# Kernel optimization log

Measured on AMD Instinct MI355X. Metric: run time of the kernel, lower is better.

The kernel has to match this reference:

```python
import jax, jax.numpy as jnp
import numpy as np

K = 20

def lrelu(x):
    return jnp.where(x >= 0, x, 0.2 * x)

def get_graph_feature(x, k):
    # x: (B, N, C) channel-last. Returns (B, N, k, 2C) = [neighbor - x, x].
    inner = jnp.einsum('bnc,bmc->bnm', x, x)          # (B, N, N)
    sq = jnp.sum(x * x, axis=-1)                       # (B, N)
    # negative squared distance; top-k gives nearest neighbors (incl. self)
    neg_dist = 2.0 * inner - sq[:, :, None] - sq[:, None, :]
    _, idx = jax.lax.top_k(neg_dist, k)                # (B, N, k)
    neigh = jnp.take_along_axis(x[:, None, :, :], idx[:, :, :, None], axis=2)  # (B, N, k, C)
    center = jnp.broadcast_to(x[:, :, None, :], neigh.shape)
    return jnp.concatenate([neigh - center, center], axis=-1)

def setup_inputs() -> dict:
    key = jax.random.key(0)
    ks = jax.random.split(key, 12)
    B, N, input_dim = 32, 2048, 6
    emb_dim, out_dim = 1024, 40
    def w(k_, shape):
        fan_in = shape[-1]
        return jax.random.normal(k_, shape, dtype=jnp.float32) * (1.0 / np.sqrt(fan_in))
    return {
        'x':  jax.random.normal(ks[0], (B, N, input_dim), dtype=jnp.float32),
        'W1': w(ks[1], (64, 6)),            # conv1: 1x1 conv, no bias
        'W2': w(ks[2], (64, 128)),          # conv2
        'W5': w(ks[3], (emb_dim, 128)),     # conv5 (1d)
        'W3': w(ks[4], (32, input_dim - 3)),# conv3
        'W4': w(ks[5], (64, 32)),           # conv4
        'L1': w(ks[6], (128, (emb_dim + 64) * 2)),  # linear1, no bias
        'L2w': w(ks[7], (64, 128)),
        'L2b': jnp.zeros((64,), dtype=jnp.float32),
        'L3w': w(ks[8], (out_dim, 64)),
        'L3b': jnp.zeros((out_dim,), dtype=jnp.float32),
    }

def reference(x, W1, W2, W5, W3, W4, L1, L2w, L2b, L3w, L3b):
    x_pos = x[:, :, :3]       # (B, N, 3)
    x_feat = x[:, :, 3:]      # (B, N, input_dim-3)

    # EdgeConv block 1
    e = get_graph_feature(x_pos, K)                       # (B, N, k, 6)
    e = lrelu(jnp.einsum('bnkc,oc->bnko', e, W1))         # (B, N, k, 64)
    x1 = jnp.max(e, axis=2)                               # (B, N, 64)

    # EdgeConv block 2
    e = get_graph_feature(x1, K)                          # (B, N, k, 128)
    e = lrelu(jnp.einsum('bnkc,oc->bnko', e, W2))         # (B, N, k, 64)
    x2 = jnp.max(e, axis=2)                               # (B, N, 64)

    # conv5 over concatenated features
    h = jnp.concatenate([x1, x2], axis=-1)                # (B, N, 128)
    h = lrelu(jnp.einsum('bnc,oc->bno', h, W5))           # (B, N, emb)
    g = jnp.concatenate([jnp.max(h, axis=1), jnp.mean(h, axis=1)], axis=-1)  # (B, 2*emb)

    # per-point feature MLP (conv3 -> conv4)
    f = lrelu(jnp.einsum('bnc,oc->bno', x_feat, W3))      # (B, N, 32)
    f = lrelu(jnp.einsum('bnc,oc->bno', f, W4))           # (B, N, 64)
    fg = jnp.concatenate([jnp.max(f, axis=1), jnp.mean(f, axis=1)], axis=-1)  # (B, 128)

    z = jnp.concatenate([g, fg], axis=-1)                 # (B, (emb+64)*2)
    z = lrelu(z @ L1.T)
    z = lrelu(z @ L2w.T + L2b)
    return z @ L3w.T + L3b                                # (B, output)
```

## Files before the change

### kernel.cpp

```cpp
#include <hip/hip_runtime.h>
#include <math.h>

#define B_ 32
#define N_ 2048
#define KNN 20
#define FINF 3.402823466e38f
#define SCAP 256

typedef __attribute__((ext_vector_type(8))) short short8;
typedef __attribute__((ext_vector_type(4))) float f32x4;

#define OFF_X1   ((size_t)0)
#define OFF_X2   (OFF_X1 + (size_t)B_*N_*64*4)
#define OFF_SQ1  (OFF_X2 + (size_t)B_*N_*64*4)
#define OFF_IDX1 (OFF_SQ1 + (size_t)B_*N_*4)
#define OFF_IDX2 (OFF_IDX1 + (size_t)B_*N_*KNN*4)
#define OFF_PMAX (OFF_IDX2 + (size_t)B_*N_*KNN*4)
#define OFF_PSUM (OFF_PMAX + (size_t)B_*16*1024*4)
#define OFF_G    (OFF_PSUM + (size_t)B_*16*1024*4)
#define OFF_FG   (OFF_G + (size_t)B_*2048*4)
#define OFF_DIST (OFF_FG + (size_t)B_*128*4)
#define OFF_BASE OFF_DIST
#define OFF_XHI  (OFF_BASE + (size_t)B_*N_*64*4)
#define OFF_XLO  (OFF_XHI + (size_t)B_*N_*128*2)
#define OFF_WHI  (OFF_XLO + (size_t)B_*N_*128*2)
#define OFF_WLO  (OFF_WHI + (size_t)1024*128*2)

__device__ __forceinline__ float lrelu(float x) { return x >= 0.0f ? x : 0.2f * x; }

template<class F>
__device__ __forceinline__ void wave_top20_slow(const float (&v)[32], int lane, int* out20, F idxf) {
    unsigned alive = 0xffffffffu;
    for (int sel = 0; sel < 20; ++sel) {
        float bv = -FINF;
        int bm = 0x7fffffff;
#pragma unroll
        for (int j = 0; j < 32; ++j) {
            bool a = (alive >> j) & 1u;
            bool better = a && (v[j] > bv);
            bv = better ? v[j] : bv;
            bm = better ? idxf(j) : bm;
        }
#pragma unroll
        for (int off = 32; off; off >>= 1) {
            float ov = __shfl_xor(bv, off, 64);
            int   om = __shfl_xor(bm, off, 64);
            bool take = (ov > bv) || (ov == bv && om < bm);
            bv = take ? ov : bv;
            bm = take ? om : bm;
        }
        if (lane == 0) out20[sel] = bm;
#pragma unroll
        for (int j = 0; j < 32; ++j)
            if (idxf(j) == bm) alive &= ~(1u << j);
    }
}

template<class F>
__device__ __forceinline__ void wave_top20_fast(const float (&v)[32], int lane,
                                                float* sval, int* sidx, int* out20, F idxf) {
    float lm = v[0];
#pragma unroll
    for (int j = 1; j < 32; ++j) lm = fmaxf(lm, v[j]);
    float s = lm;
#pragma unroll
    for (int k = 2; k <= 64; k <<= 1) {
#pragma unroll
        for (int j2 = k >> 1; j2 > 0; j2 >>= 1) {
            float o = __shfl_xor(s, j2, 64);
            bool up = ((lane & k) == 0);
            bool high = ((lane & j2) != 0);
            s = (high == up) ? fmaxf(s, o) : fminf(s, o);
        }
    }
    float that = __shfl(s, 44, 64);
    int cnt = 0;
    unsigned long long below = (lane == 63) ? 0xffffffffffffffffull >> 1
                                            : ((1ull << lane) - 1ull);
#pragma unroll
    for (int j = 0; j < 32; ++j) {
        bool p = (v[j] >= that);
        unsigned long long mk = __ballot(p);
        if (p) {
            int slot = cnt + (int)__popcll(mk & below);
            if (slot < SCAP) { sval[slot] = v[j]; sidx[slot] = idxf(j); }
        }
        cnt += (int)__popcll(mk);
    }
    int S = cnt;
    if (S > SCAP) {
        wave_top20_slow(v, lane, out20, idxf);
        return;
    }
    if (S <= 64) {
        bool ok = lane < S;
        float cv = ok ? sval[lane] : -FINF;
        int   cm = ok ? sidx[lane] : 0x7fffffff;
#pragma unroll
        for (int k = 2; k <= 64; k <<= 1) {
#pragma unroll
            for (int j2 = k >> 1; j2 > 0; j2 >>= 1) {
                float ov = __shfl_xor(cv, j2, 64);
                int   om = __shfl_xor(cm, j2, 64);
                bool up = ((lane & k) == 0);
                bool high = ((lane & j2) != 0);
                bool cur_first = (cv > ov) || (cv == ov && cm < om);
                bool take = (high == up) ? cur_first : !cur_first;
                cv = take ? ov : cv;
                cm = take ? om : cm;
            }
        }
        if (lane < 20) out20[lane] = cm;
    } else {
        float cv[4]; int cm[4]; unsigned alive = 0;
#pragma unroll
        for (int r = 0; r < 4; ++r) {
            int i = r * 64 + lane;
            bool ok = i < S;
            float vv = sval[i];
            int   mm = sidx[i];
            cv[r] = ok ? vv : -FINF;
            cm[r] = ok ? mm : 0x7fffffff;
            if (ok) alive |= 1u << r;
        }
        for (int sel = 0; sel < 20; ++sel) {
            float bv = -FINF; int bm = 0x7fffffff;
#pragma unroll
            for (int r = 0; r < 4; ++r) {
                bool a = (alive >> r) & 1u;
                bool better = a && (cv[r] > bv || (cv[r] == bv && cm[r] < bm));
                bv = better ? cv[r] : bv;
                bm = better ? cm[r] : bm;
            }
#pragma unroll
            for (int off = 32; off; off >>= 1) {
                float ov = __shfl_xor(bv, off, 64);
                int   om = __shfl_xor(bm, off, 64);
                bool take = (ov > bv) || (ov == bv && om < bm);
                bv = take ? ov : bv;
                bm = take ? om : bm;
            }
            if (lane == 0) out20[sel] = bm;
#pragma unroll
            for (int r = 0; r < 4; ++r)
                if (cm[r] == bm) alive &= ~(1u << r);
        }
    }
}

__global__ __launch_bounds__(256) void k1_knn_pos(const float* __restrict__ x,
                                                  int* __restrict__ idx1) {
    __shared__ float sP[N_ * 3];
    __shared__ float sval[4][SCAP];
    __shared__ int   sidx[4][SCAP];
    __shared__ int   sOut[4][20];
    int tid = threadIdx.x;
    int wid = tid >> 6, lane = tid & 63;
    int row = blockIdx.x * 4 + wid;
    int b = row >> 11, n = row & 2047;
    const float* xb = x + (size_t)b * N_ * 6;
    for (int m = tid; m < N_; m += 256) {
        float4 f = *(const float4*)(xb + m * 6);
        sP[m*3+0] = f.x; sP[m*3+1] = f.y; sP[m*3+2] = f.z;
    }
    __syncthreads();
    float cx = sP[n*3+0], cy = sP[n*3+1], cz = sP[n*3+2];
    float sqn = cx*cx + cy*cy + cz*cz;
    float v[32];
#pragma unroll
    for (int j = 0; j < 32; ++j) {
        int m = lane + (j << 6);
        float mx_ = sP[m*3+0], my = sP[m*3+1], mz = sP[m*3+2];
        float inner = cx*mx_ + cy*my + cz*mz;
        float sqm = mx_*mx_ + my*my + mz*mz;
        v[j] = 2.0f*inner - sqn - sqm;
    }
    wave_top20_fast(v, lane, sval[wid], sidx[wid], sOut[wid],
                    [lane](int j) { return lane + (j << 6); });
    __syncthreads();
    if (lane < 20) idx1[(size_t)row*KNN + lane] = sOut[wid][lane];
}

__global__ __launch_bounds__(256) void k2_conv1(const float* __restrict__ x,
                                                const int* __restrict__ idx1,
                                                const float* __restrict__ W1,
                                                float* __restrict__ x1,
                                                float* __restrict__ sq1) {
    int wid = threadIdx.x >> 6, o = threadIdx.x & 63;
    int row = blockIdx.x * 4 + wid;
    int b = row >> 11, n = row & 2047;
    const float* xb = x + (size_t)b * N_ * 6;
    float w0 = W1[o*6+0], w1 = W1[o*6+1], w2 = W1[o*6+2];
    float w3 = W1[o*6+3], w4 = W1[o*6+4], w5 = W1[o*6+5];
    float cx = xb[n*6+0], cy = xb[n*6+1], cz = xb[n*6+2];
    float base = w3*cx + w4*cy + w5*cz;
    float mx = -FINF;
    for (int k = 0; k < KNN; ++k) {
        int m = idx1[(size_t)row*KNN + k];
        float dx = xb[m*6+0]-cx, dy = xb[m*6+1]-cy, dz = xb[m*6+2]-cz;
        float s = base + w0*dx + w1*dy + w2*dz;
        s = lrelu(s);
        mx = fmaxf(mx, s);
    }
    x1[(size_t)row*64 + o] = mx;
    float sq = mx*mx;
#pragma unroll
    for (int off = 32; off; off >>= 1) sq += __shfl_xor(sq, off, 64);
    if (o == 0) sq1[row] = sq;
}

__global__ __launch_bounds__(256) void k3_dist(const float* __restrict__ x1,
                                               const float* __restrict__ sq1,
                                               float* __restrict__ dist, int b0) {
    __shared__ float sA[32][128];
    __shared__ float sB[32][128];
    int t = blockIdx.x;
    int I = (int)((sqrtf(8.0f*t + 1.0f) - 1.0f) * 0.5f);
    while ((I+1)*(I+2)/2 <= t) ++I;
    while (I*(I+1)/2 > t) --I;
    int J = t - I*(I+1)/2;
    int b = b0 + blockIdx.y;
    const float* Xb  = x1  + (size_t)b * N_ * 64;
    const float* sqb = sq1 + (size_t)b * N_;
    float* Db = dist + (size_t)blockIdx.y * N_ * N_;
    int i0 = I*128, j0 = J*128;
    int tid = threadIdx.x;
    float acc[8][8] = {};
    for (int kt = 0; kt < 64; kt += 32) {
#pragma unroll
        for (int l = 0; l < 4; ++l) {
            int v = l*256 + tid;
            int i = v >> 3, cg = (v & 7) << 2;
            float4 fa = *(const float4*)(Xb + (size_t)(i0+i)*64 + kt + cg);
            sA[cg+0][i] = fa.x; sA[cg+1][i] = fa.y; sA[cg+2][i] = fa.z; sA[cg+3][i] = fa.w;
            float4 fb = *(const float4*)(Xb + (size_t)(j0+i)*64 + kt + cg);
            sB[cg+0][i] = fb.x; sB[cg+1][i] = fb.y; sB[cg+2][i] = fb.z; sB[cg+3][i] = fb.w;
        }
        __syncthreads();
        int ti = (tid & 15) * 8, tj = (tid >> 4) * 8;
#pragma unroll 4
        for (int c = 0; c < 32; ++c) {
            float a[8], w[8];
            *(float4*)&a[0] = *(const float4*)&sA[c][ti];
            *(float4*)&a[4] = *(const float4*)&sA[c][ti+4];
            *(float4*)&w[0] = *(const float4*)&sB[c][tj];
            *(float4*)&w[4] = *(const float4*)&sB[c][tj+4];
#pragma unroll
            for (int ii = 0; ii < 8; ++ii)
#pragma unroll
                for (int jj = 0; jj < 8; ++jj)
                    acc[ii][jj] = fmaf(a[ii], w[jj], acc[ii][jj]);
        }
        __syncthreads();
    }
    int ti = (tid & 15) * 8, tj = (tid >> 4) * 8;
    float sqi[8], sqj[8];
#pragma unroll
    for (int ii = 0; ii < 8; ++ii) sqi[ii] = sqb[i0 + ti + ii];
#pragma unroll
    for (int jj = 0; jj < 8; ++jj) sqj[jj] = sqb[j0 + tj + jj];
#pragma unroll
    for (int ii = 0; ii < 8; ++ii) {
        float ov[8];
#pragma unroll
        for (int jj = 0; jj < 8; ++jj) ov[jj] = 2.0f*acc[ii][jj] - sqi[ii] - sqj[jj];
        float4* p = (float4*)(Db + (size_t)(i0+ti+ii)*N_ + j0 + tj);
        p[0] = *(float4*)&ov[0]; p[1] = *(float4*)&ov[4];
    }
    if (I != J) {
#pragma unroll
        for (int jj = 0; jj < 8; ++jj) {
            float ov[8];
#pragma unroll
            for (int ii = 0; ii < 8; ++ii) ov[ii] = 2.0f*acc[ii][jj] - sqi[ii] - sqj[jj];
            float4* p = (float4*)(Db + (size_t)(j0+tj+jj)*N_ + i0 + ti);
            p[0] = *(float4*)&ov[0]; p[1] = *(float4*)&ov[4];
        }
    }
}

__global__ __launch_bounds__(256) void k4_topk(const float* __restrict__ dist,
                                               int* __restrict__ idx2, int b0) {
    __shared__ float sval[4][SCAP];
    __shared__ int   sidx[4][SCAP];
    __shared__ int   sOut[4][20];
    int wid = threadIdx.x >> 6, lane = threadIdx.x & 63;
    int lrow = blockIdx.x * 4 + wid;
    int lb = lrow >> 11, n = lrow & 2047;
    const float4* Dr4 = (const float4*)(dist + (size_t)lb * N_ * N_ + (size_t)n * N_);
    float v[32];
#pragma unroll
    for (int j4 = 0; j4 < 8; ++j4) {
        float4 f = Dr4[(j4 << 6) + lane];
        v[j4*4+0] = f.x; v[j4*4+1] = f.y; v[j4*4+2] = f.z; v[j4*4+3] = f.w;
    }
    wave_top20_fast(v, lane, sval[wid], sidx[wid], sOut[wid],
                    [lane](int j) { return (lane << 2) + ((j >> 2) << 8) + (j & 3); });
    __syncthreads();
    int row = (b0 + lb) * N_ + n;
    if (lane < 20) idx2[(size_t)row*KNN + lane] = sOut[wid][lane];
}

__global__ __launch_bounds__(256) void k5pre_base(const float* __restrict__ x1,
                                                  const float* __restrict__ W2,
                                                  float* __restrict__ base) {
    int w = threadIdx.x >> 6, o = threadIdx.x & 63;
    float wreg[64];
    const float* wsrc = W2 + (size_t)o * 128 + 64;
#pragma unroll
    for (int j = 0; j < 16; ++j)
        *(float4*)&wreg[j*4] = *(const float4*)(wsrc + j*4);
    int row0 = (blockIdx.x * 4 + w) * 32;
    for (int r = 0; r < 32; ++r) {
        const float* xr = x1 + (size_t)(row0 + r) * 64;
        float acc = 0.0f;
#pragma unroll
        for (int j = 0; j < 16; ++j) {
            float4 xc = *(const float4*)(xr + j*4);
            acc = fmaf(wreg[j*4+0], xc.x, acc);
            acc = fmaf(wreg[j*4+1], xc.y, acc);
            acc = fmaf(wreg[j*4+2], xc.z, acc);
            acc = fmaf(wreg[j*4+3], xc.w, acc);
        }
        base[(size_t)(row0 + r) * 64 + o] = acc;
    }
}

__global__ __launch_bounds__(256) void k5_conv2(const float* __restrict__ x1,
                                                const int* __restrict__ idx2,
                                                const float* __restrict__ W2,
                                                const float* __restrict__ base,
                                                float* __restrict__ x2) {
    __shared__ float sWT[64][64];
    __shared__ float sD[4][20][66];
    int tid = threadIdx.x;
    int w = tid >> 6, lane = tid & 63;
    int row = blockIdx.x * 4 + w;
    int b = row >> 11, n = row & 2047;
    const float* Xb = x1 + (size_t)b * N_ * 64;
    {
        int o = tid & 63, chunk = tid >> 6;
        int c0 = chunk * 16;
        const float* src = W2 + (size_t)o * 128 + c0;
#pragma unroll
        for (int j = 0; j < 4; ++j) {
            float4 f = *(const float4*)(src + j * 4);
            int c = c0 + j * 4;
            sWT[c+0][o] = f.x; sWT[c+1][o] = f.y; sWT[c+2][o] = f.z; sWT[c+3][o] = f.w;
        }
    }
    const float* cen = Xb + (size_t)n * 64;
#pragma unroll
    for (int it = 0; it < 5; ++it) {
        int task = lane + it * 64;
        int k = task >> 4, c4 = (task & 15) * 4;
        int m = idx2[(size_t)row * KNN + k];
        float4 nb = *(const float4*)(Xb + (size_t)m * 64 + c4);
        float4 ce = *(const float4*)(cen + c4);
        float4 d;
        d.x = nb.x - ce.x; d.y = nb.y - ce.y; d.z = nb.z - ce.z; d.w = nb.w - ce.w;
        *(float4*)&sD[w][k][c4] = d;
    }
    __syncthreads();
    int og = lane & 15, kg = lane >> 4;
    int o0 = og * 4;
    float4 bs = *(const float4*)(base + (size_t)row * 64 + o0);
    float bb[4] = {bs.x, bs.y, bs.z, bs.w};
    float acc[5][4] = {};
    for (int c4 = 0; c4 < 64; c4 += 4) {
        float wv[4][4];
#pragma unroll
        for (int ci = 0; ci < 4; ++ci)
            *(float4*)wv[ci] = *(const float4*)&sWT[c4 + ci][o0];
        float dv[5][4];
#pragma unroll
        for (int ki = 0; ki < 5; ++ki)
            *(float4*)dv[ki] = *(const float4*)&sD[w][kg * 5 + ki][c4];
#pragma unroll
        for (int ki = 0; ki < 5; ++ki)
#pragma unroll
            for (int ci = 0; ci < 4; ++ci)
#pragma unroll
                for (int oi = 0; oi < 4; ++oi)
                    acc[ki][oi] = fmaf(dv[ki][ci], wv[ci][oi], acc[ki][oi]);
    }
    float res[4];
#pragma unroll
    for (int oi = 0; oi < 4; ++oi) {
        float m = -FINF;
#pragma unroll
        for (int ki = 0; ki < 5; ++ki)
            m = fmaxf(m, lrelu(bb[oi] + acc[ki][oi]));
        m = fmaxf(m, __shfl_xor(m, 16, 64));
        m = fmaxf(m, __shfl_xor(m, 32, 64));
        res[oi] = m;
    }
    if (kg == 0) {
        float4 o4; o4.x = res[0]; o4.y = res[1]; o4.z = res[2]; o4.w = res[3];
        *(float4*)(x2 + (size_t)row * 64 + o0) = o4;
    }
}

__global__ __launch_bounds__(256) void k6pre_split(const float* __restrict__ x1,
                                                   const float* __restrict__ x2,
                                                   const float* __restrict__ W5,
                                                   unsigned short* __restrict__ Xhi,
                                                   unsigned short* __restrict__ Xlo,
                                                   unsigned short* __restrict__ Whi,
                                                   unsigned short* __restrict__ Wlo) {
    const int NX = B_ * N_ * 128 / 4;
    int e4 = blockIdx.x * 256 + threadIdx.x;
    float4 v;
    unsigned short* dh; unsigned short* dl; size_t doff;
    if (e4 < NX) {
        int r = e4 >> 5, c4 = (e4 & 31) << 2;
        v = (c4 < 64) ? *(const float4*)(x1 + (size_t)r*64 + c4)
                      : *(const float4*)(x2 + (size_t)r*64 + (c4 - 64));
        dh = Xhi; dl = Xlo; doff = (size_t)r*128 + c4;
    } else {
        int e = e4 - NX;
        if (e >= 1024*128/4) return;
        int r = e >> 5, c4 = (e & 31) << 2;
        v = *(const float4*)(W5 + (size_t)r*128 + c4);
        dh = Whi; dl = Wlo; doff = (size_t)r*128 + c4;
    }
    float a[4] = {v.x, v.y, v.z, v.w};
    unsigned short hh[4], ll[4];
#pragma unroll
    for (int i = 0; i < 4; ++i) {
        unsigned u = __float_as_uint(a[i]);
        unsigned r16 = (u + 0x7fffu + ((u >> 16) & 1u)) >> 16;
        hh[i] = (unsigned short)r16;
        float lo = a[i] - __uint_as_float(r16 << 16);
        unsigned ul = __float_as_uint(lo);
        ll[i] = (unsigned short)((ul + 0x7fffu + ((ul >> 16) & 1u)) >> 16);
    }
    *(uint2*)(dh + doff) = make_uint2((unsigned)hh[0] | ((unsigned)hh[1] << 16),
                                      (unsigned)hh[2] | ((unsigned)hh[3] << 16));
    *(uint2*)(dl + doff) = make_uint2((unsigned)ll[0] | ((unsigned)ll[1] << 16),
                                      (unsigned)ll[2] | ((unsigned)ll[3] << 16));
}

__global__ __launch_bounds__(256) void k6a_mfma(const unsigned short* __restrict__ Xhi,
                                                const unsigned short* __restrict__ Xlo,
                                                const unsigned short* __restrict__ Whi,
                                                const unsigned short* __restrict__ Wlo,
                                                float* __restrict__ pmax,
                                                float* __restrict__ psum) {
    __shared__ unsigned short sT[4][128*32];
    __shared__ float redmx[128][2], redsm[128][2];
    int tid = threadIdx.x;
    int nt = blockIdx.x >> 3, ot = blockIdx.x & 7, b = blockIdx.y;
    int wid = tid >> 6, lane = tid & 63;
    int wn = wid & 1, wo = wid >> 1;
    int sub = lane & 15, quad = lane >> 4;
    const unsigned short* gp[4];
    gp[0] = Xhi + (size_t)(b*2048 + nt*128) * 128;
    gp[1] = Xlo + (size_t)(b*2048 + nt*128) * 128;
    gp[2] = Whi + (size_t)(ot*128) * 128;
    gp[3] = Wlo + (size_t)(ot*128) * 128;
    f32x4 acc[4][4];
#pragma unroll
    for (int i = 0; i < 4; ++i)
#pragma unroll
        for (int j = 0; j < 4; ++j) acc[i][j] = (f32x4)0.0f;
    for (int kt = 0; kt < 4; ++kt) {
        int k0 = kt * 32;
        __syncthreads();
#pragma unroll
        for (int it = 0; it < 8; ++it) {
            int task = it*256 + tid;
            int tile = task >> 9, rem = task & 511;
            int row = rem >> 2, ch = rem & 3;
            uint4 d = *(const uint4*)(gp[tile] + (size_t)row*128 + k0 + ch*8);
            *(uint4*)(&sT[tile][row*32 + ch*8]) = d;
        }
        __syncthreads();
        short8 ah[4], al[4], bh[4], bl[4];
#pragma unroll
        for (int mi = 0; mi < 4; ++mi) {
            int r = wn*64 + mi*16 + sub;
            ah[mi] = *(const short8*)(&sT[0][r*32 + quad*8]);
            al[mi] = *(const short8*)(&sT[1][r*32 + quad*8]);
        }
#pragma unroll
        for (int ni = 0; ni < 4; ++ni) {
            int r = wo*64 + ni*16 + sub;
            bh[ni] = *(const short8*)(&sT[2][r*32 + quad*8]);
            bl[ni] = *(const short8*)(&sT[3][r*32 + quad*8]);
        }
#pragma unroll
        for (int mi = 0; mi < 4; ++mi)
#pragma unroll
            for (int ni = 0; ni < 4; ++ni) {
                acc[mi][ni] = __builtin_amdgcn_mfma_f32_16x16x32_bf16(ah[mi], bh[ni], acc[mi][ni], 0, 0, 0);
                acc[mi][ni] = __builtin_amdgcn_mfma_f32_16x16x32_bf16(ah[mi], bl[ni], acc[mi][ni], 0, 0, 0);
                acc[mi][ni] = __builtin_amdgcn_mfma_f32_16x16x32_bf16(al[mi], bh[ni], acc[mi][ni], 0, 0, 0);
            }
    }
#pragma unroll
    for (int ni = 0; ni < 4; ++ni) {
        float mx = -FINF, sm = 0.0f;
#pragma unroll
        for (int mi = 0; mi < 4; ++mi)
#pragma unroll
            for (int r = 0; r < 4; ++r) {
                float v = lrelu(acc[mi][ni][r]);
                mx = fmaxf(mx, v); sm += v;
            }
        mx = fmaxf(mx, __shfl_xor(mx, 16, 64));
        mx = fmaxf(mx, __shfl_xor(mx, 32, 64));
        sm += __shfl_xor(sm, 16, 64);
        sm += __shfl_xor(sm, 32, 64);
        if (quad == 0) {
            redmx[wo*64 + ni*16 + sub][wn] = mx;
            redsm[wo*64 + ni*16 + sub][wn] = sm;
        }
    }
    __syncthreads();
    if (tid < 128) {
        float mx = fmaxf(redmx[tid][0], redmx[tid][1]);
        float sm = redsm[tid][0] + redsm[tid][1];
        size_t po = ((size_t)b*16 + nt)*1024 + ot*128 + tid;
        pmax[po] = mx; psum[po] = sm;
    }
}

__global__ __launch_bounds__(256) void k6b_reduce(const float* __restrict__ pmax,
                                                  const float* __restrict__ psum,
                                                  float* __restrict__ g) {
    int t = blockIdx.x * 256 + threadIdx.x;
    int b = t >> 10, o = t & 1023;
    float mx = -FINF, sm = 0.0f;
    for (int i = 0; i < 16; ++i) {
        mx = fmaxf(mx, pmax[((size_t)b*16 + i)*1024 + o]);
        sm += psum[((size_t)b*16 + i)*1024 + o];
    }
    g[(size_t)b*2048 + o] = mx;
    g[(size_t)b*2048 + 1024 + o] = sm * (1.0f/2048.0f);
}

__global__ __launch_bounds__(256) void k7_feat(const float* __restrict__ x,
                                               const float* __restrict__ W3,
                                               const float* __restrict__ W4,
                                               float* __restrict__ fg) {
    __shared__ float rmx[16*256];
    __shared__ float rsm[16*256];
    int b = blockIdx.y, og = blockIdx.x;
    int o0 = og * 16;
    int tid = threadIdx.x;
    float mx[16], sm[16];
#pragma unroll
    for (int i = 0; i < 16; ++i) { mx[i] = -FINF; sm[i] = 0.0f; }
    for (int n = tid; n < N_; n += 256) {
        const float* xr = x + ((size_t)b*N_ + n)*6 + 3;
        float f0 = xr[0], f1 = xr[1], f2 = xr[2];
        float h1[32];
#pragma unroll
        for (int j = 0; j < 32; ++j) {
            float s = W3[j*3]*f0 + W3[j*3+1]*f1 + W3[j*3+2]*f2;
            h1[j] = lrelu(s);
        }
#pragma unroll
        for (int oi = 0; oi < 16; ++oi) {
            float s = 0.0f;
#pragma unroll
            for (int j = 0; j < 32; ++j) s = fmaf(W4[(o0+oi)*32 + j], h1[j], s);
            s = lrelu(s);
            mx[oi] = fmaxf(mx[oi], s); sm[oi] += s;
        }
    }
#pragma unroll
    for (int oi = 0; oi < 16; ++oi) { rmx[oi*256 + tid] = mx[oi]; rsm[oi*256 + tid] = sm[oi]; }
    __syncthreads();
    for (int s = 128; s > 0; s >>= 1) {
        if (tid < s) {
#pragma unroll
            for (int oi = 0; oi < 16; ++oi) {
                rmx[oi*256 + tid] = fmaxf(rmx[oi*256 + tid], rmx[oi*256 + tid + s]);
                rsm[oi*256 + tid] += rsm[oi*256 + tid + s];
            }
        }
        __syncthreads();
    }
    if (tid < 16) {
        fg[(size_t)b*128 + o0 + tid]      = rmx[tid*256];
        fg[(size_t)b*128 + 64 + o0 + tid] = rsm[tid*256] * (1.0f/2048.0f);
    }
}

__global__ __launch_bounds__(128) void k8_head(const float* __restrict__ g,
                                               const float* __restrict__ fg,
                                               const float* __restrict__ L1w,
                                               const float* __restrict__ L2w,
                                               const float* __restrict__ L2b,
                                               const float* __restrict__ L3w,
                                               const float* __restrict__ L3b,
                                               float* __restrict__ out) {
    __shared__ float sz[2176];
    __shared__ float s1[128];
    __shared__ float s2[64];
    int b = blockIdx.x, tid = threadIdx.x;
    for (int c = tid; c < 2048; c += 128) sz[c] = g[(size_t)b*2048 + c];
    if (tid < 128) sz[2048 + tid] = fg[(size_t)b*128 + tid];
    __syncthreads();
    {
        float a = 0.0f;
        const float* w = L1w + (size_t)tid * 2176;
        for (int c = 0; c < 2176; ++c) a = fmaf(w[c], sz[c], a);
        s1[tid] = lrelu(a);
    }
    __syncthreads();
    if (tid < 64) {
        float a = L2b[tid];
        for (int c = 0; c < 128; ++c) a = fmaf(L2w[tid*128 + c], s1[c], a);
        s2[tid] = lrelu(a);
    }
    __syncthreads();
    if (tid < 40) {
        float a = L3b[tid];
        for (int c = 0; c < 64; ++c) a = fmaf(L3w[tid*64 + c], s2[c], a);
        out[(size_t)b*40 + tid] = a;
    }
}

extern "C" void kernel_launch(void* const* d_in, const int* in_sizes, int n_in,
                              void* d_out, int out_size, void* d_ws, size_t ws_size,
                              hipStream_t stream) {
    const float* x   = (const float*)d_in[0];
    const float* W1  = (const float*)d_in[1];
    const float* W2  = (const float*)d_in[2];
    const float* W5  = (const float*)d_in[3];
    const float* W3  = (const float*)d_in[4];
    const float* W4  = (const float*)d_in[5];
    const float* L1w = (const float*)d_in[6];
    const float* L2w = (const float*)d_in[7];
    const float* L2b = (const float*)d_in[8];
    const float* L3w = (const float*)d_in[9];
    const float* L3b = (const float*)d_in[10];
    float* out = (float*)d_out;

    char* ws = (char*)d_ws;
    float* x1   = (float*)(ws + OFF_X1);
    float* x2   = (float*)(ws + OFF_X2);
    float* sq1  = (float*)(ws + OFF_SQ1);
    int*   idx1 = (int*)  (ws + OFF_IDX1);
    int*   idx2 = (int*)  (ws + OFF_IDX2);
    float* pmax = (float*)(ws + OFF_PMAX);
    float* psum = (float*)(ws + OFF_PSUM);
    float* g    = (float*)(ws + OFF_G);
    float* fg   = (float*)(ws + OFF_FG);
    float* dist = (float*)(ws + OFF_DIST);
    float* base = (float*)(ws + OFF_BASE);
    unsigned short* Xhi = (unsigned short*)(ws + OFF_XHI);
    unsigned short* Xlo = (unsigned short*)(ws + OFF_XLO);
    unsigned short* Whi = (unsigned short*)(ws + OFF_WHI);
    unsigned short* Wlo = (unsigned short*)(ws + OFF_WLO);

    size_t distBytes = (size_t)N_ * N_ * 4;
    size_t availB = (ws_size > OFF_DIST) ? (ws_size - OFF_DIST) : 0;
    int maxcb = (int)(availB / distBytes);
    int cb = 4;
    while (cb * 2 <= maxcb && cb * 2 <= 32) cb <<= 1;

    k1_knn_pos<<<16384, 256, 0, stream>>>(x, idx1);
    k2_conv1<<<16384, 256, 0, stream>>>(x, idx1, W1, x1, sq1);
    for (int b0 = 0; b0 < 32; b0 += cb) {
        k3_dist<<<dim3(136, cb), 256, 0, stream>>>(x1, sq1, dist, b0);
        k4_topk<<<cb * 512, 256, 0, stream>>>(dist, idx2, b0);
    }
    k5pre_base<<<512, 256, 0, stream>>>(x1, W2, base);
    k5_conv2<<<16384, 256, 0, stream>>>(x1, idx2, W2, base, x2);
    k6pre_split<<<8320, 256, 0, stream>>>(x1, x2, W5, Xhi, Xlo, Whi, Wlo);
    k6a_mfma<<<dim3(128, 32), 256, 0, stream>>>(Xhi, Xlo, Whi, Wlo, pmax, psum);
    k6b_reduce<<<128, 256, 0, stream>>>(pmax, psum, g);
    k7_feat<<<dim3(4, 32), 256, 0, stream>>>(x, W3, W4, fg);
    k8_head<<<32, 128, 0, stream>>>(g, fg, L1w, L2w, L2b, L3w, L3b, out);
}
```

Before: 977.5 us.

## Factor EdgeConv2 linear map into per-point P and Q before gathering

```diff
diff --git a/kernel.cpp b/kernel.cpp
--- a/kernel.cpp
+++ b/kernel.cpp
@@ -20,10 +20,11 @@
 #define OFF_G    (OFF_PSUM + (size_t)B_*16*1024*4)
 #define OFF_FG   (OFF_G + (size_t)B_*2048*4)
 #define OFF_DIST (OFF_FG + (size_t)B_*128*4)
-#define OFF_BASE OFF_DIST
-#define OFF_XHI  (OFF_BASE + (size_t)B_*N_*64*4)
-#define OFF_XLO  (OFF_XHI + (size_t)B_*N_*128*2)
-#define OFF_WHI  (OFF_XLO + (size_t)B_*N_*128*2)
+#define OFF_P    OFF_DIST
+#define OFF_Q    (OFF_P + (size_t)B_*N_*64*4)
+#define OFF_XHI  OFF_P
+#define OFF_XLO  OFF_Q
+#define OFF_WHI  (OFF_Q + (size_t)B_*N_*64*4)
 #define OFF_WLO  (OFF_WHI + (size_t)1024*128*2)
 
 __device__ __forceinline__ float lrelu(float x) { return x >= 0.0f ? x : 0.2f * x; }
@@ -301,104 +302,57 @@
     if (lane < 20) idx2[(size_t)row*KNN + lane] = sOut[wid][lane];
 }
 
-__global__ __launch_bounds__(256) void k5pre_base(const float* __restrict__ x1,
-                                                  const float* __restrict__ W2,
-                                                  float* __restrict__ base) {
+__global__ __launch_bounds__(256) void k5pre_pq(const float* __restrict__ x1,
+                                                const float* __restrict__ W2,
+                                                float* __restrict__ P,
+                                                float* __restrict__ Q) {
     int w = threadIdx.x >> 6, o = threadIdx.x & 63;
-    float wreg[64];
-    const float* wsrc = W2 + (size_t)o * 128 + 64;
-#pragma unroll
-    for (int j = 0; j < 16; ++j)
-        *(float4*)&wreg[j*4] = *(const float4*)(wsrc + j*4);
+    float wd[64], wc[64];
+    const float* wsrc = W2 + (size_t)o * 128;
+#pragma unroll
+    for (int j = 0; j < 16; ++j) {
+        float4 d = *(const float4*)(wsrc + j*4);
+        float4 c = *(const float4*)(wsrc + 64 + j*4);
+        wd[j*4+0] = d.x; wd[j*4+1] = d.y; wd[j*4+2] = d.z; wd[j*4+3] = d.w;
+        wc[j*4+0] = c.x - d.x; wc[j*4+1] = c.y - d.y; wc[j*4+2] = c.z - d.z; wc[j*4+3] = c.w - d.w;
+    }
     int row0 = (blockIdx.x * 4 + w) * 32;
     for (int r = 0; r < 32; ++r) {
         const float* xr = x1 + (size_t)(row0 + r) * 64;
-        float acc = 0.0f;
+        float p = 0.0f, q = 0.0f;
 #pragma unroll
         for (int j = 0; j < 16; ++j) {
             float4 xc = *(const float4*)(xr + j*4);
-            acc = fmaf(wreg[j*4+0], xc.x, acc);
-            acc = fmaf(wreg[j*4+1], xc.y, acc);
-            acc = fmaf(wreg[j*4+2], xc.z, acc);
-            acc = fmaf(wreg[j*4+3], xc.w, acc);
-        }
-        base[(size_t)(row0 + r) * 64 + o] = acc;
-    }
-}
-
-__global__ __launch_bounds__(256) void k5_conv2(const float* __restrict__ x1,
-                                                const int* __restrict__ idx2,
-                                                const float* __restrict__ W2,
-                                                const float* __restrict__ base,
-                                                float* __restrict__ x2) {
-    __shared__ float sWT[64][64];
-    __shared__ float sD[4][20][66];
-    int tid = threadIdx.x;
-    int w = tid >> 6, lane = tid & 63;
+            p = fmaf(wd[j*4+0], xc.x, p); q = fmaf(wc[j*4+0], xc.x, q);
+            p = fmaf(wd[j*4+1], xc.y, p); q = fmaf(wc[j*4+1], xc.y, q);
+            p = fmaf(wd[j*4+2], xc.z, p); q = fmaf(wc[j*4+2], xc.z, q);
+            p = fmaf(wd[j*4+3], xc.w, p); q = fmaf(wc[j*4+3], xc.w, q);
+        }
+        P[(size_t)(row0 + r) * 64 + o] = p;
+        Q[(size_t)(row0 + r) * 64 + o] = q;
+    }
+}
+
+__global__ __launch_bounds__(256) void k5b_max(const float* __restrict__ P,
+                                               const float* __restrict__ Q,
+                                               const int* __restrict__ idx2,
+                                               float* __restrict__ x2) {
+    int w = threadIdx.x >> 6, lane = threadIdx.x & 63;
     int row = blockIdx.x * 4 + w;
-    int b = row >> 11, n = row & 2047;
-    const float* Xb = x1 + (size_t)b * N_ * 64;
-    {
-        int o = tid & 63, chunk = tid >> 6;
-        int c0 = chunk * 16;
-        const float* src = W2 + (size_t)o * 128 + c0;
-#pragma unroll
-        for (int j = 0; j < 4; ++j) {
-            float4 f = *(const float4*)(src + j * 4);
-            int c = c0 + j * 4;
-            sWT[c+0][o] = f.x; sWT[c+1][o] = f.y; sWT[c+2][o] = f.z; sWT[c+3][o] = f.w;
-        }
-    }
-    const float* cen = Xb + (size_t)n * 64;
-#pragma unroll
-    for (int it = 0; it < 5; ++it) {
-        int task = lane + it * 64;
-        int k = task >> 4, c4 = (task & 15) * 4;
-        int m = idx2[(size_t)row * KNN + k];
-        float4 nb = *(const float4*)(Xb + (size_t)m * 64 + c4);
-        float4 ce = *(const float4*)(cen + c4);
-        float4 d;
-        d.x = nb.x - ce.x; d.y = nb.y - ce.y; d.z = nb.z - ce.z; d.w = nb.w - ce.w;
-        *(float4*)&sD[w][k][c4] = d;
-    }
-    __syncthreads();
-    int og = lane & 15, kg = lane >> 4;
-    int o0 = og * 4;
-    float4 bs = *(const float4*)(base + (size_t)row * 64 + o0);
-    float bb[4] = {bs.x, bs.y, bs.z, bs.w};
-    float acc[5][4] = {};
-    for (int c4 = 0; c4 < 64; c4 += 4) {
-        float wv[4][4];
-#pragma unroll
-        for (int ci = 0; ci < 4; ++ci)
-            *(float4*)wv[ci] = *(const float4*)&sWT[c4 + ci][o0];
-        float dv[5][4];
-#pragma unroll
-        for (int ki = 0; ki < 5; ++ki)
-            *(float4*)dv[ki] = *(const float4*)&sD[w][kg * 5 + ki][c4];
-#pragma unroll
-        for (int ki = 0; ki < 5; ++ki)
-#pragma unroll
-            for (int ci = 0; ci < 4; ++ci)
-#pragma unroll
-                for (int oi = 0; oi < 4; ++oi)
-                    acc[ki][oi] = fmaf(dv[ki][ci], wv[ci][oi], acc[ki][oi]);
-    }
-    float res[4];
-#pragma unroll
-    for (int oi = 0; oi < 4; ++oi) {
-        float m = -FINF;
-#pragma unroll
-        for (int ki = 0; ki < 5; ++ki)
-            m = fmaxf(m, lrelu(bb[oi] + acc[ki][oi]));
-        m = fmaxf(m, __shfl_xor(m, 16, 64));
-        m = fmaxf(m, __shfl_xor(m, 32, 64));
-        res[oi] = m;
-    }
-    if (kg == 0) {
-        float4 o4; o4.x = res[0]; o4.y = res[1]; o4.z = res[2]; o4.w = res[3];
-        *(float4*)(x2 + (size_t)row * 64 + o0) = o4;
-    }
+    int b = row >> 11;
+    float q = Q[(size_t)row * 64 + lane];
+    const int* id = idx2 + (size_t)row * KNN;
+    const float* Pb = P + ((size_t)b << 11) * 64;
+    int midx[KNN];
+#pragma unroll
+    for (int k = 0; k < KNN; ++k) midx[k] = id[k];
+    float mx = -FINF;
+#pragma unroll
+    for (int k = 0; k < KNN; ++k) {
+        float p = Pb[(size_t)midx[k] * 64 + lane];
+        mx = fmaxf(mx, lrelu(p + q));
+    }
+    x2[(size_t)row * 64 + lane] = mx;
 }
 
 __global__ __launch_bounds__(256) void k6pre_split(const float* __restrict__ x1,
@@ -651,7 +605,8 @@
     float* g    = (float*)(ws + OFF_G);
     float* fg   = (float*)(ws + OFF_FG);
     float* dist = (float*)(ws + OFF_DIST);
-    float* base = (float*)(ws + OFF_BASE);
+    float* P    = (float*)(ws + OFF_P);
+    float* Q    = (float*)(ws + OFF_Q);
     unsigned short* Xhi = (unsigned short*)(ws + OFF_XHI);
     unsigned short* Xlo = (unsigned short*)(ws + OFF_XLO);
     unsigned short* Whi = (unsigned short*)(ws + OFF_WHI);
@@ -669,8 +624,8 @@
         k3_dist<<<dim3(136, cb), 256, 0, stream>>>(x1, sq1, dist, b0);
         k4_topk<<<cb * 512, 256, 0, stream>>>(dist, idx2, b0);
     }
-    k5pre_base<<<512, 256, 0, stream>>>(x1, W2, base);
-    k5_conv2<<<16384, 256, 0, stream>>>(x1, idx2, W2, base, x2);
+    k5pre_pq<<<512, 256, 0, stream>>>(x1, W2, P, Q);
+    k5b_max<<<16384, 256, 0, stream>>>(P, Q, idx2, x2);
     k6pre_split<<<8320, 256, 0, stream>>>(x1, x2, W5, Xhi, Xlo, Whi, Wlo);
     k6a_mfma<<<dim3(128, 32), 256, 0, stream>>>(Xhi, Xlo, Whi, Wlo, pmax, psum);
     k6b_reduce<<<128, 256, 0, stream>>>(pmax, psum, g);
```

After: 863.7 us. 1.13x faster.
